# Kernel optimization log

Measured on AMD Instinct MI355X. Metric: run time of the kernel, lower is better.

The kernel has to match this reference:

```python
import jax, jax.numpy as jnp
import numpy as np

B, S, V, E, H, T = 128, 512, 50000, 300, 256, 9


def setup_inputs() -> dict:
    key = jax.random.key(0)
    ks = jax.random.split(key, 20)
    def n(k, shape, s=0.1):
        return (jax.random.normal(k, shape, jnp.float32) * s).astype(jnp.float32)
    return {
        "x": jax.random.randint(ks[0], (B, S), 1, V),           # nonzero -> mask all True
        "tags": jax.random.randint(ks[1], (B, S), 0, T),
        "emb": n(ks[2], (V, E)),
        "Wih_l0f": n(ks[3], (4 * H, E)), "Whh_l0f": n(ks[4], (4 * H, H)), "b_l0f": n(ks[5], (4 * H,)),
        "Wih_l0b": n(ks[6], (4 * H, E)), "Whh_l0b": n(ks[7], (4 * H, H)), "b_l0b": n(ks[8], (4 * H,)),
        "Wih_l1f": n(ks[9], (4 * H, 2 * H)), "Whh_l1f": n(ks[10], (4 * H, H)), "b_l1f": n(ks[11], (4 * H,)),
        "Wih_l1b": n(ks[12], (4 * H, 2 * H)), "Whh_l1b": n(ks[13], (4 * H, H)), "b_l1b": n(ks[14], (4 * H,)),
        "fc_w": n(ks[15], (T, 2 * H)), "fc_b": n(ks[16], (T,)),
        "crf_start": n(ks[17], (T,)), "crf_end": n(ks[18], (T,)), "crf_trans": n(ks[19], (T, T)),
    }


def _lstm_dir(x, Wih, Whh, b, reverse):
    # x: [B,S,D] -> hidden states [B,S,H]; PyTorch gate order i,f,g,o
    Bx, Hh = x.shape[0], Whh.shape[1]
    xs = jnp.swapaxes(x, 0, 1)  # [S,B,D]
    if reverse:
        xs = xs[::-1]
    xW = xs @ Wih.T + b  # precompute input projection [S,B,4H]
    def step(carry, g_in):
        h, c = carry
        g = g_in + h @ Whh.T
        i, f, gg, o = jnp.split(g, 4, axis=-1)
        c = jax.nn.sigmoid(f) * c + jax.nn.sigmoid(i) * jnp.tanh(gg)
        h = jax.nn.sigmoid(o) * jnp.tanh(c)
        return (h, c), h
    h0 = jnp.zeros((Bx, Hh), x.dtype)
    _, hs = jax.lax.scan(step, (h0, h0), xW)
    if reverse:
        hs = hs[::-1]
    return jnp.swapaxes(hs, 0, 1)


def _crf_nll(emissions, tags, mask, start, end, trans):
    # torchcrf: llh = numerator(score of gold path) - log-partition; return mean NLL
    mf = mask.astype(emissions.dtype)
    em_tag = jnp.take_along_axis(emissions, tags[..., None], axis=2)[..., 0]  # [B,S]
    num = start[tags[:, 0]] + em_tag[:, 0]
    trans_sc = trans[tags[:, :-1], tags[:, 1:]]  # [B,S-1]
    num = num + jnp.sum((trans_sc + em_tag[:, 1:]) * mf[:, 1:], axis=1)
    last = jnp.sum(mask.astype(jnp.int32), axis=1) - 1
    last_tags = jnp.take_along_axis(tags, last[:, None], axis=1)[:, 0]
    num = num + end[last_tags]
    # forward algorithm
    alpha = start[None, :] + emissions[:, 0]  # [B,T]
    em_t = jnp.swapaxes(emissions[:, 1:], 0, 1)  # [S-1,B,T]
    m_t = jnp.swapaxes(mask[:, 1:], 0, 1)        # [S-1,B]
    def step(alpha, inp):
        em, m = inp
        nxt = jax.scipy.special.logsumexp(alpha[:, :, None] + trans[None] + em[:, None, :], axis=1)
        return jnp.where(m[:, None], nxt, alpha), None
    alpha, _ = jax.lax.scan(step, alpha, (em_t, m_t))
    denom = jax.scipy.special.logsumexp(alpha + end[None, :], axis=1)
    return jnp.mean(denom - num)


def reference(x, tags, emb, Wih_l0f, Whh_l0f, b_l0f, Wih_l0b, Whh_l0b, b_l0b,
              Wih_l1f, Whh_l1f, b_l1f, Wih_l1b, Whh_l1b, b_l1b,
              fc_w, fc_b, crf_start, crf_end, crf_trans):
    mask = (x != 0)
    e = emb[x]  # [B,S,E]
    l0 = jnp.concatenate([_lstm_dir(e, Wih_l0f, Whh_l0f, b_l0f, False),
                          _lstm_dir(e, Wih_l0b, Whh_l0b, b_l0b, True)], axis=-1)
    l1 = jnp.concatenate([_lstm_dir(l0, Wih_l1f, Whh_l1f, b_l1f, False),
                          _lstm_dir(l0, Wih_l1b, Whh_l1b, b_l1b, True)], axis=-1)
    emissions = l1 @ fc_w.T + fc_b  # [B,S,T] (dropout = identity in eval)
    return _crf_nll(emissions, tags, mask, crf_start, crf_end, crf_trans)
```

## Files before the change

### kernel.cpp

```cpp
#include <hip/hip_runtime.h>
#include <cstdint>
#include <cstddef>

#define BATCH   128
#define SEQ     512
#define TOKENS  (BATCH * SEQ)
#define EMB_D   300
#define KA0     320
#define HID     256
#define G4H     1024
#define KA1     512
#define NTAGS   9
#define CHUNK   128
#define CTOK    (BATCH * CHUNK)

#define WREG    23
#define WLDS    9

typedef _Float16 f16;
typedef _Float16 f16x2 __attribute__((ext_vector_type(2)));
typedef _Float16 f16x8 __attribute__((ext_vector_type(8)));
typedef float    f32x4 __attribute__((ext_vector_type(4)));

static constexpr size_t XW_BYTES   = (size_t)2 * CTOK * G4H * 2;
static constexpr size_t H_BYTES    = (size_t)TOKENS * KA1 * 2;
static constexpr size_t POOL_BYTES = H_BYTES;
static constexpr size_t EM_BYTES   = (size_t)TOKENS * 16 * 4;
static constexpr size_t WHH_BYTES  = (size_t)4 * G4H * HID * 2;
static constexpr size_t WIH0_BYTES = (size_t)2 * G4H * KA0 * 2;
static constexpr size_t WIH1_BYTES = (size_t)2 * G4H * KA1 * 2;
static constexpr size_t FCW_BYTES  = (size_t)128 * KA1 * 2;
static constexpr size_t FCB_BYTES  = 512;
static constexpr size_t STH_BYTES  = (size_t)2 * BATCH * HID * 2;
static constexpr size_t STC_BYTES  = (size_t)2 * BATCH * HID * 4;
static constexpr size_t NLL_BYTES  = 512;

static constexpr size_t OFF_XW   = 0;
static constexpr size_t OFF_H0   = OFF_XW   + XW_BYTES;
static constexpr size_t OFF_POOL = OFF_H0   + H_BYTES;
static constexpr size_t OFF_EM   = OFF_POOL + POOL_BYTES;
static constexpr size_t OFF_WHH  = OFF_EM   + EM_BYTES;
static constexpr size_t OFF_WIH0 = OFF_WHH  + WHH_BYTES;
static constexpr size_t OFF_WIH1 = OFF_WIH0 + WIH0_BYTES;
static constexpr size_t OFF_FCW  = OFF_WIH1 + WIH1_BYTES;
static constexpr size_t OFF_FCB  = OFF_FCW  + FCW_BYTES;
static constexpr size_t OFF_STH  = OFF_FCB  + FCB_BYTES;
static constexpr size_t OFF_STC  = OFF_STH  + STH_BYTES;
static constexpr size_t OFF_NLL  = OFF_STC  + STC_BYTES;

__device__ inline float fdot2(uint32_t a, uint32_t b, float c) {
#if __has_builtin(__builtin_amdgcn_fdot2)
  return __builtin_amdgcn_fdot2(__builtin_bit_cast(f16x2, a),
                                __builtin_bit_cast(f16x2, b), c, false);
#else
  f16x2 ha = __builtin_bit_cast(f16x2, a), hb = __builtin_bit_cast(f16x2, b);
  return c + (float)ha.x * (float)hb.x + (float)ha.y * (float)hb.y;
#endif
}

__device__ inline int swz(int r, int q) { return q ^ ((r & 3) ^ ((r >> 2) & 3)); }

__global__ void prep_kernel(
    const float* whh_l0f, const float* whh_l0b, const float* whh_l1f, const float* whh_l1b,
    const float* wih_l0f, const float* wih_l0b,
    const float* wih_l1f, const float* wih_l1b,
    const float* fc_w, const float* fc_b,
    f16* whh16, f16* wih0_16, f16* wih1_16, f16* fcw16, float* fcb32)
{
  int id = blockIdx.x * 256 + threadIdx.x;
  if (id < 1048576) {
    int which = id >> 18; int off = id & 262143;
    const float* s = which == 0 ? whh_l0f : which == 1 ? whh_l0b
                   : which == 2 ? whh_l1f : whh_l1b;
    whh16[id] = (f16)s[off];
    return;
  }
  id -= 1048576;
  if (id < 655360) {
    int dir = id / 327680; int rem = id - dir * 327680;
    int r = rem / KA0; int k = rem - r * KA0;
    const float* s = dir ? wih_l0b : wih_l0f;
    wih0_16[id] = (f16)(k < EMB_D ? s[r * EMB_D + k] : 0.f);
    return;
  }
  id -= 655360;
  if (id < 1048576) {
    const float* s = (id < 524288) ? wih_l1f : wih_l1b;
    wih1_16[id] = (f16)s[id & 524287];
    return;
  }
  id -= 1048576;
  if (id < 65536) {
    int r = id >> 9;
    fcw16[id] = (f16)(r < NTAGS ? fc_w[id] : 0.f);
    return;
  }
  id -= 65536;
  if (id < 128) fcb32[id] = id < NTAGS ? fc_b[id] : 0.f;
}

__global__ void embed_kernel(const int* __restrict__ x, const float* __restrict__ emb,
                             f16* __restrict__ e16)
{
  int id = blockIdx.x * 256 + threadIdx.x;
  if (id >= TOKENS * KA0) return;
  int row = id / KA0, k = id - row * KA0;
  float v = 0.f;
  if (k < EMB_D) v = emb[(size_t)x[row] * EMB_D + k];
  e16[id] = (f16)v;
}

__global__ __launch_bounds__(256, 3) void gemm_kernel(
    const f16* __restrict__ A, int lda, int aGrpStride,
    const f16* __restrict__ B0, const f16* __restrict__ B1, int ldb,
    const float* __restrict__ bias0, const float* __restrict__ bias1,
    f16* outH, float* outF, int ldc, size_t outZStride,
    int kChunks, int nLimit, int cbF, int cbB)
{
  __shared__ __align__(16) f16 As[128 * 32];
  __shared__ __align__(16) f16 Bs[128 * 32];
  const int z = blockIdx.z;
  const f16* B = z ? B1 : B0;
  const float* bias = z ? bias1 : bias0;
  const int cb = z ? cbB : cbF;
  const int m0 = blockIdx.x * 128, n0 = blockIdx.y * 128;
  const int aBase = (m0 >> 7) * aGrpStride + cb;
  const int tid = threadIdx.x;
  const int w = tid >> 6, lane = tid & 63;
  const int mw = (w & 1) * 64, nw = (w >> 1) * 64;
  const int fr = lane & 15, fq = lane >> 4;

  f32x4 acc[4][4];
#pragma unroll
  for (int i = 0; i < 4; ++i)
#pragma unroll
    for (int j = 0; j < 4; ++j) acc[i][j] = (f32x4)(0.f);

  const int c0 = tid, c1 = tid + 256;
  const int r0 = c0 >> 2, q0 = c0 & 3, r1c = c1 >> 2, q1 = c1 & 3;

  for (int kc = 0; kc < kChunks; ++kc) {
    const int k0 = kc * 32;
    uint4 a0v = *(const uint4*)(A + (size_t)(aBase + r0)  * lda + k0 + q0 * 8);
    uint4 a1v = *(const uint4*)(A + (size_t)(aBase + r1c) * lda + k0 + q1 * 8);
    uint4 b0v = *(const uint4*)(B + (size_t)(n0 + r0)  * ldb + k0 + q0 * 8);
    uint4 b1v = *(const uint4*)(B + (size_t)(n0 + r1c) * ldb + k0 + q1 * 8);
    __syncthreads();
    *(uint4*)(As + r0  * 32 + swz(r0,  q0) * 8) = a0v;
    *(uint4*)(As + r1c * 32 + swz(r1c, q1) * 8) = a1v;
    *(uint4*)(Bs + r0  * 32 + swz(r0,  q0) * 8) = b0v;
    *(uint4*)(Bs + r1c * 32 + swz(r1c, q1) * 8) = b1v;
    __syncthreads();
    f16x8 af[4], bf[4];
#pragma unroll
    for (int i = 0; i < 4; ++i) {
      int rr = mw + i * 16 + fr;
      af[i] = *(const f16x8*)(As + rr * 32 + swz(rr, fq) * 8);
    }
#pragma unroll
    for (int j = 0; j < 4; ++j) {
      int rr = nw + j * 16 + fr;
      bf[j] = *(const f16x8*)(Bs + rr * 32 + swz(rr, fq) * 8);
    }
#pragma unroll
    for (int i = 0; i < 4; ++i)
#pragma unroll
      for (int j = 0; j < 4; ++j)
        acc[i][j] = __builtin_amdgcn_mfma_f32_16x16x32_f16(af[i], bf[j], acc[i][j], 0, 0, 0);
  }
  f16* oH = outH ? outH + (size_t)z * outZStride : nullptr;
  float* oF = outF;
#pragma unroll
  for (int j = 0; j < 4; ++j) {
    int n = n0 + nw + j * 16 + fr;
    if (n >= nLimit) continue;
    float bs = bias ? bias[n] : 0.f;
#pragma unroll
    for (int i = 0; i < 4; ++i) {
#pragma unroll
      for (int r = 0; r < 4; ++r) {
        int m = m0 + mw + i * 16 + fq * 4 + r;
        float v = acc[i][j][r] + bs;
        if (oH) oH[(size_t)m * ldc + n] = (f16)v;
        else    oF[(size_t)m * ldc + n] = v;
      }
    }
  }
}

__global__ __launch_bounds__(1024, 4) void rec_kernel(
    const f16* __restrict__ xw,
    const uint32_t* __restrict__ whh_f, const uint32_t* __restrict__ whh_b,
    f16* __restrict__ hout,
    f16* __restrict__ stateH, float* __restrict__ stateC, int r)
{
  __shared__ __align__(16) uint4 wlds[WLDS * 1024];
  __shared__ float gates[1024];
  __shared__ __align__(16) f16 hbuf[2][256];
  const int tau = threadIdx.x;
  const int bid = blockIdx.x;
  const int dir = bid >> 7;
  const int b   = bid & 127;
  const int chunk = dir ? (3 - r) : r;
  const int tBase = chunk * CHUNK;
  const uint32_t* whh = dir ? whh_b : whh_f;
  const f16* xwp = xw + (size_t)(dir * 128 + b) * CHUNK * 1024;

  uint4 wa4[WREG];
  {
    const uint4* p0 = (const uint4*)(whh + tau * 128);
#pragma unroll
    for (int i = 0; i < WREG; ++i) wa4[i] = p0[i];
#pragma unroll
    for (int c = 0; c < WLDS; ++c) wlds[c * 1024 + tau] = p0[WREG + c];
  }
  float cst = 0.f;
  if (tau < 256) {
    f16 hi = (f16)0.f;
    if (r) { hi = stateH[(dir * 128 + b) * 256 + tau]; cst = stateC[(dir * 128 + b) * 256 + tau]; }
    hbuf[0][tau] = hi;
  }
  __syncthreads();

  int lr0 = dir ? (CHUNK - 1) : 0;
  f16 xw_cur = xwp[lr0 * 1024 + tau];

  for (int s = 0; s < CHUNK; ++s) {
    const int lrow = dir ? (CHUNK - 1 - s) : s;
    const size_t token = (size_t)b * 512 + tBase + lrow;
    const int cur = s & 1, nxt = cur ^ 1;
    f16 xw_nextv = (f16)0.f;
    if (s < CHUNK - 1) {
      int lrn = dir ? (CHUNK - 2 - s) : (s + 1);
      xw_nextv = xwp[lrn * 1024 + tau];
    }
    float a0 = (float)xw_cur;
    const uint4* hb4 = (const uint4*)hbuf[cur];
#pragma unroll
    for (int c = 0; c < WLDS; ++c) {
      uint4 hv = hb4[WREG + c];
      uint4 wv = wlds[c * 1024 + tau];
      a0 = fdot2(wv.x, hv.x, a0);
      a0 = fdot2(wv.y, hv.y, a0);
      a0 = fdot2(wv.z, hv.z, a0);
      a0 = fdot2(wv.w, hv.w, a0);
    }
#pragma unroll
    for (int i = 0; i < WREG; ++i) {
      uint4 hv = hb4[i];
      a0 = fdot2(wa4[i].x, hv.x, a0);
      a0 = fdot2(wa4[i].y, hv.y, a0);
      a0 = fdot2(wa4[i].z, hv.z, a0);
      a0 = fdot2(wa4[i].w, hv.w, a0);
    }
    gates[tau] = a0;
    __syncthreads();
    if (tau < 256) {
      float gi = gates[tau], gf = gates[256 + tau], gg = gates[512 + tau], go = gates[768 + tau];
      float si = 1.f / (1.f + __expf(-gi));
      float sf = 1.f / (1.f + __expf(-gf));
      float so = 1.f / (1.f + __expf(-go));
      float e2 = __expf(2.f * gg); float tg = 1.f - 2.f / (e2 + 1.f);
      cst = sf * cst + si * tg;
      e2 = __expf(2.f * cst); float tc = 1.f - 2.f / (e2 + 1.f);
      float h = so * tc;
      f16 hh = (f16)h;
      hbuf[nxt][tau] = hh;
      hout[token * 512 + dir * 256 + tau] = hh;
    }
    __syncthreads();
    xw_cur = xw_nextv;
  }
  if (tau < 256) {
    stateH[(dir * 128 + b) * 256 + tau] = hbuf[0][tau];
    stateC[(dir * 128 + b) * 256 + tau] = cst;
  }
}

__global__ void crf_kernel(const float* __restrict__ em, const int* __restrict__ tags,
                           const float* __restrict__ start, const float* __restrict__ endv,
                           const float* __restrict__ trans, float* __restrict__ nll)
{
  const int b = blockIdx.x;
  const int lane = threadIdx.x;
  const float* emb_ = em + (size_t)b * SEQ * 16;
  const int* tg = tags + b * SEQ;

  float numacc = 0.f;
  for (int t = lane; t < SEQ; t += 64) {
    int ct = tg[t];
    numacc += emb_[t * 16 + ct];
    if (t > 0) numacc += trans[tg[t - 1] * NTAGS + ct];
  }
#pragma unroll
  for (int s = 32; s; s >>= 1) numacc += __shfl_xor(numacc, s);

  int jj = lane < NTAGS ? lane : 0;
  float tr[NTAGS];
#pragma unroll
  for (int i = 0; i < NTAGS; ++i) tr[i] = trans[i * NTAGS + jj];
  float alpha = (lane < NTAGS) ? (start[lane] + emb_[lane]) : -1e30f;
  for (int t = 1; t < SEQ; ++t) {
    float va[NTAGS];
#pragma unroll
    for (int i = 0; i < NTAGS; ++i) va[i] = __shfl(alpha, i) + tr[i];
    float mx = va[0];
#pragma unroll
    for (int i = 1; i < NTAGS; ++i) mx = fmaxf(mx, va[i]);
    float s = 0.f;
#pragma unroll
    for (int i = 0; i < NTAGS; ++i) s += __expf(va[i] - mx);
    float na = mx + __logf(s) + emb_[t * 16 + jj];
    alpha = (lane < NTAGS) ? na : -1e30f;
  }
  float v = (lane < NTAGS) ? alpha + endv[lane] : -1e30f;
  float mx = v;
#pragma unroll
  for (int s2 = 32; s2; s2 >>= 1) mx = fmaxf(mx, __shfl_xor(mx, s2));
  float se = __expf(v - mx);
#pragma unroll
  for (int s2 = 32; s2; s2 >>= 1) se += __shfl_xor(se, s2);
  float denom = mx + __logf(se);
  if (lane == 0) {
    float num = numacc + start[tg[0]] + endv[tg[SEQ - 1]];
    nll[b] = denom - num;
  }
}

__global__ void reduce_kernel(const float* __restrict__ nll, float* __restrict__ out) {
  int lane = threadIdx.x;
  float v = nll[lane] + nll[lane + 64];
#pragma unroll
  for (int s = 32; s; s >>= 1) v += __shfl_xor(v, s);
  if (lane == 0) out[0] = v * (1.f / 128.f);
}

extern "C" void kernel_launch(void* const* d_in, const int* in_sizes, int n_in,
                              void* d_out, int out_size, void* d_ws, size_t ws_size,
                              hipStream_t stream)
{
  const int*   x        = (const int*)d_in[0];
  const int*   tags     = (const int*)d_in[1];
  const float* emb      = (const float*)d_in[2];
  const float* wih_l0f  = (const float*)d_in[3];
  const float* whh_l0f  = (const float*)d_in[4];
  const float* b_l0f    = (const float*)d_in[5];
  const float* wih_l0b  = (const float*)d_in[6];
  const float* whh_l0b  = (const float*)d_in[7];
  const float* b_l0b    = (const float*)d_in[8];
  const float* wih_l1f  = (const float*)d_in[9];
  const float* whh_l1f  = (const float*)d_in[10];
  const float* b_l1f    = (const float*)d_in[11];
  const float* wih_l1b  = (const float*)d_in[12];
  const float* whh_l1b  = (const float*)d_in[13];
  const float* b_l1b    = (const float*)d_in[14];
  const float* fc_w     = (const float*)d_in[15];
  const float* fc_b     = (const float*)d_in[16];
  const float* crf_start= (const float*)d_in[17];
  const float* crf_end  = (const float*)d_in[18];
  const float* crf_trans= (const float*)d_in[19];

  char* ws = (char*)d_ws;
  f16*   xw16   = (f16*)(ws + OFF_XW);
  f16*   h0     = (f16*)(ws + OFF_H0);
  f16*   e16    = (f16*)(ws + OFF_POOL);
  f16*   h1     = (f16*)(ws + OFF_POOL);
  float* em32   = (float*)(ws + OFF_EM);
  f16*   whh16  = (f16*)(ws + OFF_WHH);
  f16*   wih016 = (f16*)(ws + OFF_WIH0);
  f16*   wih116 = (f16*)(ws + OFF_WIH1);
  f16*   fcw16  = (f16*)(ws + OFF_FCW);
  float* fcb32  = (float*)(ws + OFF_FCB);
  f16*   stH    = (f16*)(ws + OFF_STH);
  float* stC    = (float*)(ws + OFF_STC);
  float* nllbuf = (float*)(ws + OFF_NLL);
  const uint32_t* whh32 = (const uint32_t*)whh16;

  prep_kernel<<<11009, 256, 0, stream>>>(whh_l0f, whh_l0b, whh_l1f, whh_l1b,
                                         wih_l0f, wih_l0b, wih_l1f, wih_l1b,
                                         fc_w, fc_b, whh16, wih016, wih116, fcw16, fcb32);
  embed_kernel<<<(TOKENS * KA0) / 256, 256, 0, stream>>>(x, emb, e16);

  const size_t zstr = (size_t)CTOK * G4H;
  dim3 gch(CTOK / 128, G4H / 128, 2);

  for (int r = 0; r < 4; ++r) {
    gemm_kernel<<<gch, 256, 0, stream>>>(e16, KA0, SEQ,
                                         wih016, wih016 + (size_t)G4H * KA0, KA0,
                                         b_l0f, b_l0b, xw16, nullptr, G4H, zstr,
                                         KA0 / 32, G4H, r * CHUNK, (3 - r) * CHUNK);
    rec_kernel<<<256, 1024, 0, stream>>>(xw16, whh32, whh32 + (size_t)G4H * 128,
                                         h0, stH, stC, r);
  }

  for (int r = 0; r < 4; ++r) {
    gemm_kernel<<<gch, 256, 0, stream>>>(h0, KA1, SEQ,
                                         wih116, wih116 + (size_t)G4H * KA1, KA1,
                                         b_l1f, b_l1b, xw16, nullptr, G4H, zstr,
                                         KA1 / 32, G4H, r * CHUNK, (3 - r) * CHUNK);
    rec_kernel<<<256, 1024, 0, stream>>>(xw16, whh32 + (size_t)2 * G4H * 128,
                                         whh32 + (size_t)3 * G4H * 128,
                                         h1, stH, stC, r);
  }

  dim3 gfc(TOKENS / 128, 1, 1);
  gemm_kernel<<<gfc, 256, 0, stream>>>(h1, KA1, 128,
                                       fcw16, nullptr, KA1, fcb32, nullptr,
                                       nullptr, em32, 16, 0, KA1 / 32, 16, 0, 0);

  crf_kernel<<<BATCH, 64, 0, stream>>>(em32, tags, crf_start, crf_end, crf_trans, nllbuf);
  reduce_kernel<<<1, 64, 0, stream>>>(nllbuf, (float*)d_out);
}
```

Measured before the change: 2.997 ms.

## Split recurrent matvec over K across four thread groups with register-resident weights

The recurrent LSTM kernel now has each thread hold a K-slice of 64 weights for all four gates of one hidden unit, entirely in registers, instead of a full 256-wide row split between registers and LDS. Partial sums are written to shared memory as float4 and reduced by the 256 gate threads, which also add the input projection. This removes the per-step LDS weight reads and makes each thread read only a quarter of h, at the cost of an extra reduction pass through LDS. The launch-bounds occupancy hint is dropped and the register footprint changes.

```diff
diff --git a/kernel.cpp b/kernel.cpp
--- a/kernel.cpp
+++ b/kernel.cpp
@@ -13,9 +13,6 @@
 #define NTAGS   9
 #define CHUNK   128
 #define CTOK    (BATCH * CHUNK)
-
-#define WREG    23
-#define WLDS    9
 
 typedef _Float16 f16;
 typedef _Float16 f16x2 __attribute__((ext_vector_type(2)));
@@ -188,16 +185,17 @@
   }
 }
 
-__global__ __launch_bounds__(1024, 4) void rec_kernel(
+__global__ __launch_bounds__(1024) void rec_kernel(
     const f16* __restrict__ xw,
     const uint32_t* __restrict__ whh_f, const uint32_t* __restrict__ whh_b,
     f16* __restrict__ hout,
     f16* __restrict__ stateH, float* __restrict__ stateC, int r)
 {
-  __shared__ __align__(16) uint4 wlds[WLDS * 1024];
-  __shared__ float gates[1024];
-  __shared__ __align__(16) f16 hbuf[2][256];
+  __shared__ __align__(16) uint4 hb[2][32];
+  __shared__ __align__(16) f32x4 part[1024];
   const int tau = threadIdx.x;
+  const int n   = tau & 255;
+  const int ks  = tau >> 8;
   const int bid = blockIdx.x;
   const int dir = bid >> 7;
   const int b   = bid & 127;
@@ -206,57 +204,66 @@
   const uint32_t* whh = dir ? whh_b : whh_f;
   const f16* xwp = xw + (size_t)(dir * 128 + b) * CHUNK * 1024;
 
-  uint4 wa4[WREG];
-  {
-    const uint4* p0 = (const uint4*)(whh + tau * 128);
-#pragma unroll
-    for (int i = 0; i < WREG; ++i) wa4[i] = p0[i];
-#pragma unroll
-    for (int c = 0; c < WLDS; ++c) wlds[c * 1024 + tau] = p0[WREG + c];
+  uint4 wv[4][8];
+#pragma unroll
+  for (int g = 0; g < 4; ++g) {
+    const uint4* p = (const uint4*)(whh) + (size_t)(g * 256 + n) * 32 + ks * 8;
+#pragma unroll
+    for (int i = 0; i < 8; ++i) wv[g][i] = p[i];
   }
   float cst = 0.f;
   if (tau < 256) {
     f16 hi = (f16)0.f;
     if (r) { hi = stateH[(dir * 128 + b) * 256 + tau]; cst = stateC[(dir * 128 + b) * 256 + tau]; }
-    hbuf[0][tau] = hi;
+    ((f16*)hb[0])[tau] = hi;
   }
   __syncthreads();
 
-  int lr0 = dir ? (CHUNK - 1) : 0;
-  f16 xw_cur = xwp[lr0 * 1024 + tau];
+  f16 xc0 = (f16)0.f, xc1 = (f16)0.f, xc2 = (f16)0.f, xc3 = (f16)0.f;
+  if (ks == 0) {
+    int lr0 = dir ? (CHUNK - 1) : 0;
+    const f16* q = xwp + lr0 * 1024;
+    xc0 = q[n]; xc1 = q[256 + n]; xc2 = q[512 + n]; xc3 = q[768 + n];
+  }
 
   for (int s = 0; s < CHUNK; ++s) {
     const int lrow = dir ? (CHUNK - 1 - s) : s;
     const size_t token = (size_t)b * 512 + tBase + lrow;
     const int cur = s & 1, nxt = cur ^ 1;
-    f16 xw_nextv = (f16)0.f;
-    if (s < CHUNK - 1) {
+    f16 xn0 = (f16)0.f, xn1 = (f16)0.f, xn2 = (f16)0.f, xn3 = (f16)0.f;
+    if (ks == 0 && s < CHUNK - 1) {
       int lrn = dir ? (CHUNK - 2 - s) : (s + 1);
-      xw_nextv = xwp[lrn * 1024 + tau];
-    }
-    float a0 = (float)xw_cur;
-    const uint4* hb4 = (const uint4*)hbuf[cur];
-#pragma unroll
-    for (int c = 0; c < WLDS; ++c) {
-      uint4 hv = hb4[WREG + c];
-      uint4 wv = wlds[c * 1024 + tau];
-      a0 = fdot2(wv.x, hv.x, a0);
-      a0 = fdot2(wv.y, hv.y, a0);
-      a0 = fdot2(wv.z, hv.z, a0);
-      a0 = fdot2(wv.w, hv.w, a0);
-    }
-#pragma unroll
-    for (int i = 0; i < WREG; ++i) {
-      uint4 hv = hb4[i];
-      a0 = fdot2(wa4[i].x, hv.x, a0);
-      a0 = fdot2(wa4[i].y, hv.y, a0);
-      a0 = fdot2(wa4[i].z, hv.z, a0);
-      a0 = fdot2(wa4[i].w, hv.w, a0);
-    }
-    gates[tau] = a0;
+      const f16* q = xwp + lrn * 1024;
+      xn0 = q[n]; xn1 = q[256 + n]; xn2 = q[512 + n]; xn3 = q[768 + n];
+    }
+    uint4 hv[8];
+    {
+      const uint4* hp = hb[cur] + ks * 8;
+#pragma unroll
+      for (int i = 0; i < 8; ++i) hv[i] = hp[i];
+    }
+    float a0 = 0.f, a1 = 0.f, a2 = 0.f, a3 = 0.f;
+#pragma unroll
+    for (int i = 0; i < 8; ++i) {
+      uint4 h4 = hv[i];
+      a0 = fdot2(wv[0][i].x, h4.x, a0); a0 = fdot2(wv[0][i].y, h4.y, a0);
+      a0 = fdot2(wv[0][i].z, h4.z, a0); a0 = fdot2(wv[0][i].w, h4.w, a0);
+      a1 = fdot2(wv[1][i].x, h4.x, a1); a1 = fdot2(wv[1][i].y, h4.y, a1);
+      a1 = fdot2(wv[1][i].z, h4.z, a1); a1 = fdot2(wv[1][i].w, h4.w, a1);
+      a2 = fdot2(wv[2][i].x, h4.x, a2); a2 = fdot2(wv[2][i].y, h4.y, a2);
+      a2 = fdot2(wv[2][i].z, h4.z, a2); a2 = fdot2(wv[2][i].w, h4.w, a2);
+      a3 = fdot2(wv[3][i].x, h4.x, a3); a3 = fdot2(wv[3][i].y, h4.y, a3);
+      a3 = fdot2(wv[3][i].w, h4.w, a3); a3 = fdot2(wv[3][i].z, h4.z, a3);
+    }
+    f32x4 pk; pk[0] = a0; pk[1] = a1; pk[2] = a2; pk[3] = a3;
+    part[tau] = pk;
     __syncthreads();
     if (tau < 256) {
-      float gi = gates[tau], gf = gates[256 + tau], gg = gates[512 + tau], go = gates[768 + tau];
+      f32x4 p0 = part[n], p1 = part[256 + n], p2 = part[512 + n], p3 = part[768 + n];
+      float gi = p0[0] + p1[0] + p2[0] + p3[0] + (float)xc0;
+      float gf = p0[1] + p1[1] + p2[1] + p3[1] + (float)xc1;
+      float gg = p0[2] + p1[2] + p2[2] + p3[2] + (float)xc2;
+      float go = p0[3] + p1[3] + p2[3] + p3[3] + (float)xc3;
       float si = 1.f / (1.f + __expf(-gi));
       float sf = 1.f / (1.f + __expf(-gf));
       float so = 1.f / (1.f + __expf(-go));
@@ -265,14 +272,14 @@
       e2 = __expf(2.f * cst); float tc = 1.f - 2.f / (e2 + 1.f);
       float h = so * tc;
       f16 hh = (f16)h;
-      hbuf[nxt][tau] = hh;
+      ((f16*)hb[nxt])[tau] = hh;
       hout[token * 512 + dir * 256 + tau] = hh;
     }
     __syncthreads();
-    xw_cur = xw_nextv;
+    xc0 = xn0; xc1 = xn1; xc2 = xn2; xc3 = xn3;
   }
   if (tau < 256) {
-    stateH[(dir * 128 + b) * 256 + tau] = hbuf[0][tau];
+    stateH[(dir * 128 + b) * 256 + tau] = ((f16*)hb[0])[tau];
     stateC[(dir * 128 + b) * 256 + tau] = cst;
   }
 }
```

Measured after the change: 5.830 ms. +94.5%, slower.
